# Performance work log

Measured on AMD Instinct MI355X. Metric: run time of the kernel, lower is better.

The kernel has to match this reference:

```python
import jax, jax.numpy as jnp
import numpy as np
from jax import lax

DN = ('NCHW', 'OIHW', 'NCHW')

def _conv(x, w, b, stride):
    y = lax.conv_general_dilated(x, w, (stride, stride), [(1, 1), (1, 1)], dimension_numbers=DN)
    return y + b[None, :, None, None]

def _deconv(x, w, b):
    # ConvTranspose2d(k=4, stride=2, pad=1) == conv with lhs_dilation=2, pad=k-1-p=2,
    # with w already in flipped OIHW layout.
    y = lax.conv_general_dilated(x, w, (1, 1), [(2, 2), (2, 2)], lhs_dilation=(2, 2), dimension_numbers=DN)
    return y + b[None, :, None, None]

def setup_inputs() -> dict:
    key = jax.random.key(0)
    ks = jax.random.split(key, 14)
    s = 0.05  # keep activations numerically tame
    return {
        'x':   jax.random.normal(ks[0], (16, 3, 256, 256), jnp.float32),
        'ew1': jax.random.normal(ks[1], (64, 3, 4, 4), jnp.float32) * s,
        'eb1': jax.random.normal(ks[2], (64,), jnp.float32) * s,
        'ew2': jax.random.normal(ks[3], (128, 64, 4, 4), jnp.float32) * s,
        'eb2': jax.random.normal(ks[4], (128,), jnp.float32) * s,
        'ew3': jax.random.normal(ks[5], (256, 128, 4, 4), jnp.float32) * s,
        'eb3': jax.random.normal(ks[6], (256,), jnp.float32) * s,
        'cb':  jax.random.normal(ks[7], (8192, 256), jnp.float32),
        'dw1': jax.random.normal(ks[8], (128, 256, 4, 4), jnp.float32) * s,
        'db1': jax.random.normal(ks[9], (128,), jnp.float32) * s,
        'dw2': jax.random.normal(ks[10], (64, 128, 4, 4), jnp.float32) * s,
        'db2': jax.random.normal(ks[11], (64,), jnp.float32) * s,
        'dw3': jax.random.normal(ks[12], (3, 64, 4, 4), jnp.float32) * s,
        'db3': jax.random.normal(ks[13], (3,), jnp.float32) * s,
    }

def reference(x, ew1, eb1, ew2, eb2, ew3, eb3, cb, dw1, db1, dw2, db2, dw3, db3):
    # encoder: 3 stride-2 convs with ReLU between
    h = jax.nn.relu(_conv(x, ew1, eb1, 2))
    h = jax.nn.relu(_conv(h, ew2, eb2, 2))
    feat = _conv(h, ew3, eb3, 2)                     # [B, 256, 32, 32]
    B, C, H, W = feat.shape
    flat = feat.reshape(B, C, H * W).transpose(0, 2, 1)  # [B, HW, C]
    scores = jnp.einsum('btc,kc->btk', flat, cb)     # [B, HW, K] large matrix
    indices = jnp.argmax(scores, axis=-1)            # [B, HW]
    quantized = cb[indices]                          # [B, HW, C]
    q = quantized.transpose(0, 2, 1).reshape(B, C, H, W)
    # decoder: 3 stride-2 transposed convs with ReLU between
    d = jax.nn.relu(_deconv(q, dw1, db1))
    d = jax.nn.relu(_deconv(d, dw2, db2))
    recon = _deconv(d, dw3, db3)                     # [B, 3, 256, 256]
    return recon, indices
```

## Files before the change

### kernel.cpp

```cpp
#include <hip/hip_runtime.h>
#include <hip/hip_fp16.h>
#include <cstdint>
#include <cstddef>

typedef __attribute__((ext_vector_type(8))) short short8;
typedef __attribute__((ext_vector_type(8))) _Float16 h16x8;
typedef __attribute__((ext_vector_type(4))) float f32x4;

__device__ __forceinline__ short f2bf(float x) {
  union { float f; unsigned u; } a; a.f = x;
  unsigned r = a.u + 0x7fff + ((a.u >> 16) & 1);
  return (short)(r >> 16);
}
__device__ __forceinline__ float bf2f(short s) {
  union { unsigned u; float f; } a;
  a.u = ((unsigned)(unsigned short)s) << 16; return a.f;
}
__device__ __forceinline__ void fsplit16(float v, short& h, short& l) {
  __half a = __float2half(v);
  h = (short)__half_as_ushort(a);
  l = (short)__half_as_ushort(__float2half(v - __half2float(a)));
}

__device__ __forceinline__ void ld16(const void* g, void* l) {
  __builtin_amdgcn_global_load_lds(
      (const __attribute__((address_space(1))) unsigned int*)g,
      (__attribute__((address_space(3))) unsigned int*)l, 16, 0, 0);
}

__global__ __launch_bounds__(256) void conv1_kernel(
    const float* __restrict__ x, const float* __restrict__ w,
    const float* __restrict__ bias, short* __restrict__ yh, short* __restrict__ yl)
{
  __shared__ __align__(16) float wl[64 * 48];
  __shared__ float bl[64];
  const int tid = threadIdx.x;
  for (int i = tid; i < 64 * 48; i += 256) wl[i] = w[i];
  if (tid < 64) bl[tid] = bias[tid];
  __syncthreads();
  const int n  = blockIdx.y;
  const int oh = blockIdx.x * 2 + (tid >> 7);
  const int ow = tid & 127;
  const float* xb = x + (size_t)n * 3 * 65536;
  const int ih0 = oh * 2 - 1, iw0 = ow * 2 - 1;
  float xin[48];
#pragma unroll
  for (int ic = 0; ic < 3; ++ic)
#pragma unroll
    for (int kh = 0; kh < 4; ++kh) {
      int ih = ih0 + kh;
      bool rok = (unsigned)ih < 256u;
#pragma unroll
      for (int kw = 0; kw < 4; ++kw) {
        int iw = iw0 + kw;
        xin[ic * 16 + kh * 4 + kw] =
            (rok && (unsigned)iw < 256u) ? xb[ic * 65536 + ih * 256 + iw] : 0.f;
      }
    }
  const size_t ob = ((size_t)n * 16384 + oh * 128 + ow) * 64;
  for (int g = 0; g < 8; ++g) {
    short hs[8], ls[8];
#pragma unroll
    for (int j = 0; j < 8; ++j) {
      const int oc = g * 8 + j;
      float acc = bl[oc];
      const float* wo = &wl[oc * 48];
#pragma unroll
      for (int t = 0; t < 48; ++t) acc = fmaf(wo[t], xin[t], acc);
      acc = fmaxf(acc, 0.f) * 64.f;
      fsplit16(acc, hs[j], ls[j]);
    }
    *(short8*)(yh + ob + g * 8) = *(short8*)hs;
    *(short8*)(yl + ob + g * 8) = *(short8*)ls;
  }
}

template <int COUT, int CIN>
__global__ __launch_bounds__(256) void wpack_conv(
    const float* __restrict__ w, short* __restrict__ Wh, short* __restrict__ Wl)
{
  constexpr int K = 16 * CIN;
  const int idx = blockIdx.x * 256 + threadIdx.x;
  const int oc = idx / K, k = idx - oc * K;
  const int kk = k / CIN, ic = k - kk * CIN;
  const int kh = kk >> 2, kw = kk & 3;
  float v = w[(((size_t)oc * CIN + ic) * 4 + kh) * 4 + kw] * 64.f;
  short h, l;
  fsplit16(v, h, l);
  Wh[idx] = h;
  Wl[idx] = l;
}

template <int CIN, int HIN, int COUTT, bool RELU, bool OUTF>
__global__ __launch_bounds__(256) void conv_mfma(
    const short* __restrict__ inh, const short* __restrict__ inl,
    const short* __restrict__ Wph, const short* __restrict__ Wpl,
    const float* __restrict__ bias,
    short* __restrict__ outh, short* __restrict__ outl,
    float* __restrict__ outf)
{
  constexpr int K = 16 * CIN;
  constexpr int HOUT = HIN / 2;
  constexpr int MT = 128, NPX = 128;
  constexpr int GS = (HOUT == 64) ? 6 : 5;
  constexpr int AE = 4 * MT;
  constexpr int NS = K / 32;
  constexpr float RS = 1.f / 4096.f;
  __shared__ __align__(16) short AhL[2][AE * 8];
  __shared__ __align__(16) short AlL[2][AE * 8];
  __shared__ __align__(16) float bl[MT];
  const int tid = threadIdx.x;
  const int w = tid >> 6, lane = tid & 63;
  const int wm = w >> 1, wn = w & 1;
  const int kgl = lane >> 4, cl = lane & 15;
  const int n = blockIdx.z;
  const int oc0 = blockIdx.y * MT;
  const int oh0 = blockIdx.x * (NPX / HOUT);
  if (tid < MT) bl[tid] = bias[oc0 + tid];

  f32x4 acc[4][4];
#pragma unroll
  for (int i = 0; i < 4; ++i)
#pragma unroll
    for (int j = 0; j < 4; ++j) acc[i][j] = (f32x4){0.f, 0.f, 0.f, 0.f};

  auto stageA = [&](int s, int b) {
    const int kc = s * 32;
#pragma unroll
    for (int rep = 0; rep < AE / 256; ++rep) {
      int e = rep * 256 + tid;
      int kg = e >> 7, oc_l = e & (MT - 1);
      size_t go = (size_t)(oc0 + oc_l) * K + kc + kg * 8;
      int lo = (e & ~63) * 8;
      ld16(Wph + go, &AhL[b][lo]);
      ld16(Wpl + go, &AlL[b][lo]);
    }
  };
  const h16x8 zzh = {0, 0, 0, 0, 0, 0, 0, 0};
  auto loadB = [&](int s, h16x8* bh, h16x8* blv) {
    const int kc = s * 32;
    const int kk = kc / CIN, ic0 = kc % CIN;
    const int kh = kk >> 2, kw = kk & 3;
#pragma unroll
    for (int nt = 0; nt < 4; ++nt) {
      int m = wn * 64 + nt * 16 + cl;
      int ih = 2 * (oh0 + (m >> GS)) - 1 + kh;
      int iw = 2 * (m & (HOUT - 1)) - 1 + kw;
      bool ok = ((unsigned)ih < (unsigned)HIN) && ((unsigned)iw < (unsigned)HIN);
      size_t go = ok ? ((size_t)((n * HIN + ih) * HIN + iw) * CIN + ic0 + kgl * 8)
                     : (size_t)(ic0 + kgl * 8);
      h16x8 vh = *(const h16x8*)(inh + go);
      h16x8 vl = *(const h16x8*)(inl + go);
      bh[nt] = ok ? vh : zzh;
      blv[nt] = ok ? vl : zzh;
    }
  };
  auto compute = [&](int b, const h16x8* bh, const h16x8* blv) {
    h16x8 ah[4], al[4];
#pragma unroll
    for (int mt = 0; mt < 4; ++mt) {
      int row = kgl * MT + wm * 64 + mt * 16 + cl;
      ah[mt] = *(const h16x8*)&AhL[b][row * 8];
      al[mt] = *(const h16x8*)&AlL[b][row * 8];
    }
#pragma unroll
    for (int mt = 0; mt < 4; ++mt)
#pragma unroll
      for (int nt = 0; nt < 4; ++nt) {
        acc[mt][nt] = __builtin_amdgcn_mfma_f32_16x16x32_f16(
            ah[mt], bh[nt], acc[mt][nt], 0, 0, 0);
        acc[mt][nt] = __builtin_amdgcn_mfma_f32_16x16x32_f16(
            ah[mt], blv[nt], acc[mt][nt], 0, 0, 0);
        acc[mt][nt] = __builtin_amdgcn_mfma_f32_16x16x32_f16(
            al[mt], bh[nt], acc[mt][nt], 0, 0, 0);
      }
  };

  h16x8 bhA[4], blA[4], bhB[4], blB[4];
  stageA(0, 0);
  loadB(0, bhA, blA);
  __syncthreads();
  for (int s2 = 0; s2 < NS; s2 += 2) {
    stageA(s2 + 1, 1);
    loadB(s2 + 1, bhB, blB);
    compute(0, bhA, blA);
    __syncthreads();
    if (s2 + 2 < NS) { stageA(s2 + 2, 0); loadB(s2 + 2, bhA, blA); }
    compute(1, bhB, blB);
    __syncthreads();
  }
#pragma unroll
  for (int mt = 0; mt < 4; ++mt) {
    const int oc = wm * 64 + mt * 16 + kgl * 4;
    const float4 bv = *(const float4*)&bl[oc];
#pragma unroll
    for (int nt = 0; nt < 4; ++nt) {
      const int px = wn * 64 + nt * 16 + cl;
      const int oh = oh0 + (px >> GS), ow = px & (HOUT - 1);
      const size_t ob =
          ((size_t)n * (HOUT * HOUT) + oh * HOUT + ow) * COUTT + oc0 + oc;
      float v0 = acc[mt][nt][0] * RS + bv.x;
      float v1 = acc[mt][nt][1] * RS + bv.y;
      float v2 = acc[mt][nt][2] * RS + bv.z;
      float v3 = acc[mt][nt][3] * RS + bv.w;
      if (RELU) {
        v0 = fmaxf(v0, 0.f); v1 = fmaxf(v1, 0.f);
        v2 = fmaxf(v2, 0.f); v3 = fmaxf(v3, 0.f);
      }
      if constexpr (OUTF) {
        ushort4 s;
        s.x = __half_as_ushort(__float2half(v0));
        s.y = __half_as_ushort(__float2half(v1));
        s.z = __half_as_ushort(__float2half(v2));
        s.w = __half_as_ushort(__float2half(v3));
        *(ushort4*)((unsigned short*)outh + ob) = s;
        *(float4*)(outf + ob) = make_float4(v0, v1, v2, v3);
      } else {
        short4 hh, ll;
        fsplit16(v0 * 64.f, hh.x, ll.x);
        fsplit16(v1 * 64.f, hh.y, ll.y);
        fsplit16(v2 * 64.f, hh.z, ll.z);
        fsplit16(v3 * 64.f, hh.w, ll.w);
        *(short4*)(outh + ob) = hh;
        *(short4*)(outl + ob) = ll;
      }
    }
  }
}

__global__ __launch_bounds__(256) void cb_convert(
    const float* __restrict__ cb, short* __restrict__ cbh,
    short* __restrict__ cbl, short* __restrict__ cb16)
{
  const int g = blockIdx.x * 256 + threadIdx.x;
  const float* p = cb + (size_t)g * 8;
  short hs[8], ls[8], fs[8];
#pragma unroll
  for (int u = 0; u < 8; ++u) {
    float v = p[u];
    short h = f2bf(v);
    hs[u] = h;
    ls[u] = f2bf(v - bf2f(h));
    fs[u] = (short)__half_as_ushort(__float2half(v));
  }
  *(short8*)(cbh + (size_t)g * 8) = *(short8*)hs;
  *(short8*)(cbl + (size_t)g * 8) = *(short8*)ls;
  *(short8*)(cb16 + (size_t)g * 8) = *(short8*)fs;
}

__global__ __launch_bounds__(256) void vq_mfma(
    const short* __restrict__ cb16, const short* __restrict__ ft16,
    float2* __restrict__ pval, int2* __restrict__ pidx)
{
  __shared__ __align__(16) short Ah[2][4 * 128 * 8];
  __shared__ __align__(16) short Bh[2][4 * 128 * 8];
  const int tid = threadIdx.x;
  const int w = tid >> 6, lane = tid & 63;
  const int wm = w >> 1, wn = w & 1;
  const int tg = blockIdx.x, cg = blockIdx.y;
  const int code0 = cg * 128, tok0 = tg * 128;
  const int kgl = lane >> 4, cl = lane & 15;

  f32x4 acc[4][4];
#pragma unroll
  for (int i = 0; i < 4; ++i)
#pragma unroll
    for (int j = 0; j < 4; ++j) acc[i][j] = (f32x4){0.f, 0.f, 0.f, 0.f};

  const int i0 = w * 128;
  auto stage = [&](int s, int b) {
    const int kc = s * 32;
#pragma unroll
    for (int rep = 0; rep < 2; ++rep) {
      int ib = i0 + rep * 64;
      int i = ib + lane;
      int m = i & 127, kg = i >> 7;
      size_t goffA = (size_t)(code0 + m) * 256 + kc + kg * 8;
      size_t goffB = (size_t)(tok0 + m) * 256 + kc + kg * 8;
      int loff = ib * 8;
      ld16(cb16 + goffA, &Ah[b][loff]);
      ld16(ft16 + goffB, &Bh[b][loff]);
    }
  };
  auto compute = [&](int b) {
    h16x8 ah[4], bh[4];
#pragma unroll
    for (int mt = 0; mt < 4; ++mt) {
      int row = wm * 64 + mt * 16 + cl;
      ah[mt] = *(const h16x8*)&Ah[b][(kgl * 128 + row) * 8];
    }
#pragma unroll
    for (int nt = 0; nt < 4; ++nt) {
      int row = wn * 64 + nt * 16 + cl;
      bh[nt] = *(const h16x8*)&Bh[b][(kgl * 128 + row) * 8];
    }
#pragma unroll
    for (int mt = 0; mt < 4; ++mt)
#pragma unroll
      for (int nt = 0; nt < 4; ++nt)
        acc[mt][nt] = __builtin_amdgcn_mfma_f32_16x16x32_f16(
            ah[mt], bh[nt], acc[mt][nt], 0, 0, 0);
  };

  stage(0, 0);
  __syncthreads();
  for (int s2 = 0; s2 < 8; s2 += 2) {
    stage(s2 + 1, 1);
    compute(0);
    __syncthreads();
    if (s2 + 2 < 8) stage(s2 + 2, 0);
    compute(1);
    __syncthreads();
  }

  float* Sv = (float*)&Ah[0][0];
  int* Si = (int*)&Bh[0][0];
#pragma unroll
  for (int nt = 0; nt < 4; ++nt) {
    float v1 = -3.4e38f, v2 = -3.4e38f;
    int j1 = 0, j2 = 0;
#pragma unroll
    for (int mt = 0; mt < 4; ++mt) {
      int cb2 = code0 + wm * 64 + mt * 16 + kgl * 4;
      f32x4 a = acc[mt][nt];
#pragma unroll
      for (int r = 0; r < 4; ++r) {
        float val = a[r];
        int code = cb2 + r;
        if (val > v1) { v2 = v1; j2 = j1; v1 = val; j1 = code; }
        else if (val > v2) { v2 = val; j2 = code; }
      }
    }
    for (int mk = 16; mk < 64; mk <<= 1) {
      float ov1 = __shfl_xor(v1, mk);
      int oj1 = __shfl_xor(j1, mk);
      float ov2 = __shfl_xor(v2, mk);
      int oj2 = __shfl_xor(j2, mk);
      if (ov1 > v1) {
        if (v1 >= ov2) { v2 = v1; j2 = j1; } else { v2 = ov2; j2 = oj2; }
        v1 = ov1; j1 = oj1;
      } else if (ov1 > v2) { v2 = ov1; j2 = oj1; }
    }
    if (lane < 16) {
      int tl = wn * 64 + nt * 16 + lane;
      Sv[(wm * 128 + tl) * 2 + 0] = v1;
      Sv[(wm * 128 + tl) * 2 + 1] = v2;
      Si[(wm * 128 + tl) * 2 + 0] = j1;
      Si[(wm * 128 + tl) * 2 + 1] = j2;
    }
  }
  __syncthreads();
  if (tid < 128) {
    int tl = tid;
    float v1 = Sv[tl * 2], v2 = Sv[tl * 2 + 1];
    int j1 = Si[tl * 2], j2 = Si[tl * 2 + 1];
    float ov1 = Sv[(128 + tl) * 2], ov2 = Sv[(128 + tl) * 2 + 1];
    int oj1 = Si[(128 + tl) * 2], oj2 = Si[(128 + tl) * 2 + 1];
    if (ov1 > v1) {
      if (v1 >= ov2) { v2 = v1; j2 = j1; } else { v2 = ov2; j2 = oj2; }
      v1 = ov1; j1 = oj1;
    } else if (ov1 > v2) { v2 = ov1; j2 = oj1; }
    size_t o = (size_t)cg * 16384 + tok0 + tl;
    pval[o] = make_float2(v1, v2);
    pidx[o] = make_int2(j1, j2);
  }
}

__global__ __launch_bounds__(256) void vq_rescore(
    const float2* __restrict__ pval, const int2* __restrict__ pidx,
    const float* __restrict__ featc, const float* __restrict__ cb,
    int* __restrict__ fidx, float* __restrict__ idx_out)
{
  const int t = blockIdx.x * 256 + threadIdx.x;
  float vs[4] = {-3.4e38f, -3.4e38f, -3.4e38f, -3.4e38f};
  int is[4] = {0, 0, 0, 0};
  for (int cgi = 0; cgi < 64; ++cgi) {
    float2 pv = pval[(size_t)cgi * 16384 + t];
    int2 pi = pidx[(size_t)cgi * 16384 + t];
#pragma unroll
    for (int s = 0; s < 2; ++s) {
      float v = s ? pv.y : pv.x;
      int ii = s ? pi.y : pi.x;
      if (v > vs[3]) {
        vs[3] = v; is[3] = ii;
#pragma unroll
        for (int k = 3; k > 0; --k)
          if (vs[k] > vs[k - 1]) {
            float tv = vs[k]; vs[k] = vs[k - 1]; vs[k - 1] = tv;
            int ti = is[k]; is[k] = is[k - 1]; is[k - 1] = ti;
          }
      }
    }
  }
  const float4* fc = (const float4*)(featc + (size_t)t * 256);
  const float4* c0 = (const float4*)(cb + (size_t)is[0] * 256);
  const float4* c1 = (const float4*)(cb + (size_t)is[1] * 256);
  const float4* c2 = (const float4*)(cb + (size_t)is[2] * 256);
  const float4* c3 = (const float4*)(cb + (size_t)is[3] * 256);
  float s0 = 0.f, s1 = 0.f, s2 = 0.f, s3 = 0.f;
  for (int k4 = 0; k4 < 64; ++k4) {
    float4 f = fc[k4];
    float4 w0 = c0[k4], w1 = c1[k4], w2 = c2[k4], w3 = c3[k4];
    s0 = fmaf(w0.x, f.x, fmaf(w0.y, f.y, fmaf(w0.z, f.z, fmaf(w0.w, f.w, s0))));
    s1 = fmaf(w1.x, f.x, fmaf(w1.y, f.y, fmaf(w1.z, f.z, fmaf(w1.w, f.w, s1))));
    s2 = fmaf(w2.x, f.x, fmaf(w2.y, f.y, fmaf(w2.z, f.z, fmaf(w2.w, f.w, s2))));
    s3 = fmaf(w3.x, f.x, fmaf(w3.y, f.y, fmaf(w3.z, f.z, fmaf(w3.w, f.w, s3))));
  }
  float best = s0; int bi = is[0];
  float sv[3] = {s1, s2, s3};
  int si2[3] = {is[1], is[2], is[3]};
#pragma unroll
  for (int c = 0; c < 3; ++c)
    if (sv[c] > best || (sv[c] == best && si2[c] < bi)) { best = sv[c]; bi = si2[c]; }
  fidx[t] = bi;
  idx_out[t] = (float)bi;
}

template <int COUT, int CIN>
__global__ __launch_bounds__(256) void wpack(
    const float* __restrict__ w, short* __restrict__ Ah, short* __restrict__ Al)
{
  constexpr int K = 4 * CIN;
  const int idx = blockIdx.x * 256 + threadIdx.x;
  const int par = idx / (COUT * K);
  const int rem = idx % (COUT * K);
  const int oc = rem / K;
  const int k = rem % K;
  const int kk = k / CIN, ic = k % CIN;
  const int kh = 2 * (kk >> 1) + (par >> 1);
  const int kw = 2 * (kk & 1) + (par & 1);
  float v = w[(((size_t)oc * CIN + ic) * 4 + kh) * 4 + kw];
  short h = f2bf(v);
  Ah[idx] = h;
  Al[idx] = f2bf(v - bf2f(h));
}

__global__ __launch_bounds__(256) void gather2(
    const short* __restrict__ cbh, const short* __restrict__ cbl,
    const int* __restrict__ fidx, short* __restrict__ qTh, short* __restrict__ qTl)
{
  const int tid = threadIdx.x;
  const int gt = blockIdx.x * 64 + (tid >> 2);
  const int part = tid & 3;
  const int code = fidx[gt];
  const short8* sh = (const short8*)(cbh + (size_t)code * 256 + part * 64);
  const short8* sl = (const short8*)(cbl + (size_t)code * 256 + part * 64);
  short8* dh = (short8*)(qTh + (size_t)gt * 256 + part * 64);
  short8* dl = (short8*)(qTl + (size_t)gt * 256 + part * 64);
#pragma unroll
  for (int j = 0; j < 8; ++j) { dh[j] = sh[j]; dl[j] = sl[j]; }
}

template <int CIN, int GRID, int COUT, int NPX, int WM, int WN, bool OUT_HALF>
__global__ __launch_bounds__(256) void deconv_mfma(
    const short* __restrict__ inh, const short* __restrict__ inl,
    const short* __restrict__ Aph, const short* __restrict__ Apl,
    const float* __restrict__ bias, void* __restrict__ out_h,
    void* __restrict__ out_l)
{
  constexpr int K = 4 * CIN, HOUT = 2 * GRID, AE = 4 * COUT;
  constexpr int GS = (GRID == 32) ? 5 : 6;
  constexpr int NS = K / 32;
  __shared__ __align__(16) short AhL[2][AE * 8];
  __shared__ __align__(16) short AlL[2][AE * 8];
  __shared__ float bl[COUT];
  const int tid = threadIdx.x;
  const int w = tid >> 6, lane = tid & 63;
  const int wm = w / WN, wn = w % WN;
  const int kgl = lane >> 4, cl = lane & 15;
  const int par = blockIdx.y, n = blockIdx.z;
  const int pr = par >> 1, pc = par & 1;
  const int Ut0 = blockIdx.x * (NPX / GRID);
  if (tid < COUT) bl[tid] = bias[tid];

  f32x4 acc[4][4];
#pragma unroll
  for (int i = 0; i < 4; ++i)
#pragma unroll
    for (int j = 0; j < 4; ++j) acc[i][j] = (f32x4){0.f, 0.f, 0.f, 0.f};

  auto stageA = [&](int s, int b) {
    const int kc = s * 32;
#pragma unroll
    for (int rep = 0; rep < AE / 256; ++rep) {
      int e = rep * 256 + tid;
      int kg = e / COUT, oc_l = e % COUT;
      size_t go = ((size_t)(par * COUT + oc_l)) * K + kc + kg * 8;
      int lo = (e & ~63) * 8;
      ld16(Aph + go, &AhL[b][lo]);
      ld16(Apl + go, &AlL[b][lo]);
    }
  };
  const short8 zz = {0, 0, 0, 0, 0, 0, 0, 0};
  auto loadB = [&](int s, short8* bh, short8* blo) {
    const int kc = s * 32;
    const int kk = kc / CIN, ic0 = kc % CIN;
    const int dr = (kk >> 1) + pr - 1, dc = (kk & 1) + pc - 1;
#pragma unroll
    for (int nt = 0; nt < 4; ++nt) {
      int m = wn * 64 + nt * 16 + cl;
      int sU = Ut0 + (m >> GS) + dr;
      int sV = (m & (GRID - 1)) + dc;
      bool ok = (unsigned)sU < (unsigned)GRID && (unsigned)sV < (unsigned)GRID;
      long pix = (long)(n * GRID + sU) * GRID + sV;
      size_t go = ok ? (size_t)(pix * CIN + ic0 + kgl * 8)
                     : (size_t)(ic0 + kgl * 8);
      short8 vh = *(const short8*)(inh + go);
      short8 vl = *(const short8*)(inl + go);
      bh[nt] = ok ? vh : zz;
      blo[nt] = ok ? vl : zz;
    }
  };
  auto compute = [&](int b, const short8* bh, const short8* blo) {
    short8 ah[4], al[4];
#pragma unroll
    for (int mt = 0; mt < 4; ++mt) {
      int row = kgl * COUT + wm * 64 + mt * 16 + cl;
      ah[mt] = *(const short8*)&AhL[b][row * 8];
      al[mt] = *(const short8*)&AlL[b][row * 8];
    }
#pragma unroll
    for (int mt = 0; mt < 4; ++mt)
#pragma unroll
      for (int nt = 0; nt < 4; ++nt) {
        acc[mt][nt] = __builtin_amdgcn_mfma_f32_16x16x32_bf16(
            ah[mt], bh[nt], acc[mt][nt], 0, 0, 0);
        acc[mt][nt] = __builtin_amdgcn_mfma_f32_16x16x32_bf16(
            ah[mt], blo[nt], acc[mt][nt], 0, 0, 0);
        acc[mt][nt] = __builtin_amdgcn_mfma_f32_16x16x32_bf16(
            al[mt], bh[nt], acc[mt][nt], 0, 0, 0);
      }
  };

  short8 bhA[4], blA[4], bhB[4], blB[4];
  stageA(0, 0);
  loadB(0, bhA, blA);
  __syncthreads();
  for (int s2 = 0; s2 < NS; s2 += 2) {
    stageA(s2 + 1, 1);
    loadB(s2 + 1, bhB, blB);
    compute(0, bhA, blA);
    __syncthreads();
    if (s2 + 2 < NS) { stageA(s2 + 2, 0); loadB(s2 + 2, bhA, blA); }
    compute(1, bhB, blB);
    __syncthreads();
  }
#pragma unroll
  for (int mt = 0; mt < 4; ++mt) {
    const int oc = wm * 64 + mt * 16 + kgl * 4;
    const float4 bv = *(const float4*)&bl[oc];
#pragma unroll
    for (int nt = 0; nt < 4; ++nt) {
      const int px = wn * 64 + nt * 16 + cl;
      const int U = Ut0 + (px >> GS), V = px & (GRID - 1);
      const int r = 2 * U + pr, c = 2 * V + pc;
      const size_t ob = ((size_t)n * HOUT * HOUT + (size_t)r * HOUT + c) * COUT + oc;
      float v0 = fmaxf(acc[mt][nt][0] + bv.x, 0.f);
      float v1 = fmaxf(acc[mt][nt][1] + bv.y, 0.f);
      float v2 = fmaxf(acc[mt][nt][2] + bv.z, 0.f);
      float v3 = fmaxf(acc[mt][nt][3] + bv.w, 0.f);
      if constexpr (OUT_HALF) {
        ushort4 s;
        s.x = __half_as_ushort(__float2half(v0));
        s.y = __half_as_ushort(__float2half(v1));
        s.z = __half_as_ushort(__float2half(v2));
        s.w = __half_as_ushort(__float2half(v3));
        *(ushort4*)((unsigned short*)out_h + ob) = s;
      } else {
        short4 hh, ll;
        hh.x = f2bf(v0); ll.x = f2bf(v0 - bf2f(hh.x));
        hh.y = f2bf(v1); ll.y = f2bf(v1 - bf2f(hh.y));
        hh.z = f2bf(v2); ll.z = f2bf(v2 - bf2f(hh.z));
        hh.w = f2bf(v3); ll.w = f2bf(v3 - bf2f(hh.w));
        *(short4*)((short*)out_h + ob) = hh;
        *(short4*)((short*)out_l + ob) = ll;
      }
    }
  }
}

__global__ __launch_bounds__(256) void deconv3_kernel(
    const __half* __restrict__ d2, const float* __restrict__ w,
    const float* __restrict__ bias, float* __restrict__ y)
{
  __shared__ __align__(16) float Xl[108 * 68];
  __shared__ __align__(16) float wl[4 * 4 * 3 * 64];
  const int tid = threadIdx.x;
  for (int i = tid; i < 3072; i += 256) {
    int oc = i >> 10, ic = (i >> 4) & 63, kh = (i >> 2) & 3, kw = i & 3;
    int par = (kh & 1) * 2 + (kw & 1), kidx = (kh >> 1) * 2 + (kw >> 1);
    wl[((par * 4 + kidx) * 3 + oc) * 64 + ic] = w[i];
  }
  const int n = blockIdx.z, r0 = blockIdx.y * 8, c0 = blockIdx.x * 32;
  const int gr0 = (r0 >> 1) - 1, gc0 = (c0 >> 1) - 1;
  for (int e = tid; e < 1728; e += 256) {
    int pl = e >> 4, sub = e & 15;
    int rr = pl / 18, cc = pl - rr * 18;
    int gr = gr0 + rr, gc = gc0 + cc;
    float4 v = make_float4(0.f, 0.f, 0.f, 0.f);
    if ((unsigned)gr < 128u && (unsigned)gc < 128u) {
      const __half2* p =
          (const __half2*)(d2 + ((size_t)(n * 16384 + gr * 128 + gc) * 64 + sub * 4));
      float2 f0 = __half22float2(p[0]);
      float2 f1 = __half22float2(p[1]);
      v = make_float4(f0.x, f0.y, f1.x, f1.y);
    }
    *(float4*)&Xl[pl * 68 + sub * 4] = v;
  }
  __syncthreads();
  const int wv = tid >> 6, lane = tid & 63;
  const int pr = wv >> 1, pc = wv & 1;
  const int Ul = lane >> 4, Vl = lane & 15;
  float a0 = bias[0], a1 = bias[1], a2 = bias[2];
  const int parb = wv * 768;
#pragma unroll
  for (int ic4 = 0; ic4 < 16; ++ic4) {
    float4 xv[4];
#pragma unroll
    for (int t = 0; t < 4; ++t) {
      int lr = Ul + (t >> 1) + pr, lc = Vl + (t & 1) + pc;
      xv[t] = *(const float4*)&Xl[(lr * 18 + lc) * 68 + ic4 * 4];
    }
#pragma unroll
    for (int t = 0; t < 4; ++t) {
      float4 w0 = *(const float4*)&wl[parb + (t * 3 + 0) * 64 + ic4 * 4];
      float4 w1 = *(const float4*)&wl[parb + (t * 3 + 1) * 64 + ic4 * 4];
      float4 w2 = *(const float4*)&wl[parb + (t * 3 + 2) * 64 + ic4 * 4];
      a0 = fmaf(w0.x, xv[t].x, fmaf(w0.y, xv[t].y, fmaf(w0.z, xv[t].z, fmaf(w0.w, xv[t].w, a0))));
      a1 = fmaf(w1.x, xv[t].x, fmaf(w1.y, xv[t].y, fmaf(w1.z, xv[t].z, fmaf(w1.w, xv[t].w, a1))));
      a2 = fmaf(w2.x, xv[t].x, fmaf(w2.y, xv[t].y, fmaf(w2.z, xv[t].z, fmaf(w2.w, xv[t].w, a2))));
    }
  }
  const int r = r0 + 2 * Ul + pr, c = c0 + 2 * Vl + pc;
  float* yn = y + (size_t)n * 3 * 65536 + r * 256 + c;
  yn[0] = a0;
  yn[65536] = a1;
  yn[131072] = a2;
}

extern "C" void kernel_launch(void* const* d_in, const int* in_sizes, int n_in,
                              void* d_out, int out_size, void* d_ws, size_t ws_size,
                              hipStream_t stream)
{
  const float* x   = (const float*)d_in[0];
  const float* ew1 = (const float*)d_in[1];
  const float* eb1 = (const float*)d_in[2];
  const float* ew2 = (const float*)d_in[3];
  const float* eb2 = (const float*)d_in[4];
  const float* ew3 = (const float*)d_in[5];
  const float* eb3 = (const float*)d_in[6];
  const float* cb  = (const float*)d_in[7];
  const float* dw1 = (const float*)d_in[8];
  const float* db1 = (const float*)d_in[9];
  const float* dw2 = (const float*)d_in[10];
  const float* db2 = (const float*)d_in[11];
  const float* dw3 = (const float*)d_in[12];
  const float* db3 = (const float*)d_in[13];

  float* recon = (float*)d_out;
  float* idxf  = (float*)d_out + 3145728;

  const size_t MB = 1048576ull;
  char* ws = (char*)d_ws;
  short* h1h = (short*)ws;
  short* h1l = (short*)(ws + 32 * MB);
  short* h2h = (short*)(ws + 64 * MB);
  short* h2l = (short*)(ws + 80 * MB);
  short* ft16  = (short*)ws;
  float* featf = (float*)(ws + 16 * MB);
  short* cbh  = (short*)(ws + 64 * MB);
  short* cbl  = (short*)(ws + 68 * MB);
  short* cb16 = (short*)(ws + 72 * MB);
  float2* pval = (float2*)(ws + 76 * MB);
  int2*   pidx = (int2*)(ws + 84 * MB);
  int*    fidx = (int*)(ws + 92 * MB);
  short* A1h = (short*)(ws + 76 * MB);
  short* A1l = (short*)(ws + 77 * MB);
  short* A2h = (short*)(ws + 78 * MB);
  short* A2l = (short*)(ws + 78 * MB + 262144);
  short* qTh = (short*)ws;
  short* qTl = (short*)(ws + 8 * MB);
  short* d1h = (short*)(ws + 32 * MB);
  short* d1l = (short*)(ws + 48 * MB);
  __half* d2 = (__half*)ws;
  short* W2h = (short*)recon;
  short* W2l = W2h + 131072;
  short* W3h = W2h + 262144;
  short* W3l = W2h + 786432;

  conv1_kernel<<<dim3(64, 16), 256, 0, stream>>>(x, ew1, eb1, h1h, h1l);
  wpack_conv<128, 64><<<dim3(512), 256, 0, stream>>>(ew2, W2h, W2l);
  conv_mfma<64, 128, 128, true, false><<<dim3(32, 1, 16), 256, 0, stream>>>(
      h1h, h1l, W2h, W2l, eb2, h2h, h2l, nullptr);
  wpack_conv<256, 128><<<dim3(2048), 256, 0, stream>>>(ew3, W3h, W3l);
  conv_mfma<128, 64, 256, false, true><<<dim3(8, 2, 16), 256, 0, stream>>>(
      h2h, h2l, W3h, W3l, eb3, ft16, nullptr, featf);

  cb_convert<<<dim3(1024), 256, 0, stream>>>(cb, cbh, cbl, cb16);
  vq_mfma<<<dim3(128, 64), 256, 0, stream>>>(cb16, ft16, pval, pidx);
  vq_rescore<<<dim3(64), 256, 0, stream>>>(pval, pidx, featf, cb, fidx, idxf);

  wpack<128, 256><<<dim3(2048), 256, 0, stream>>>(dw1, A1h, A1l);
  wpack<64, 128><<<dim3(512), 256, 0, stream>>>(dw2, A2h, A2l);
  gather2<<<dim3(256), 256, 0, stream>>>(cbh, cbl, fidx, qTh, qTl);

  deconv_mfma<256, 32, 128, 128, 2, 2, false>
      <<<dim3(8, 4, 16), 256, 0, stream>>>(qTh, qTl, A1h, A1l, db1, d1h, d1l);
  deconv_mfma<128, 64, 64, 256, 1, 4, true>
      <<<dim3(16, 4, 16), 256, 0, stream>>>(d1h, d1l, A2h, A2l, db2, d2, d2);
  deconv3_kernel<<<dim3(8, 32, 16), 256, 0, stream>>>(d2, dw3, db3, recon);
}
```

Measured before the change: 917.0 us.

## Loop each VQ block over eight codebook tiles and keep running top-4 candidates

The VQ scoring kernel now launches 8 codebook splits instead of 64. Each block walks 8 tiles of 128 codes with a continuous double-buffered pipeline and keeps a per-thread running top-2 across tiles. Each block emits top-4 candidates per token, and the rescore kernel merges only 8 partial lists instead of 64. This cuts partial-result traffic and merge work, and amortizes block startup and the final shuffle reduction. In exchange the grid has 1024 blocks instead of 8192, which lowers parallelism, and the per-thread top-2 could drop close candidates before rescoring.

```diff
diff --git a/kernel.cpp b/kernel.cpp
--- a/kernel.cpp
+++ b/kernel.cpp
@@ -250,25 +250,21 @@
 
 __global__ __launch_bounds__(256) void vq_mfma(
     const short* __restrict__ cb16, const short* __restrict__ ft16,
-    float2* __restrict__ pval, int2* __restrict__ pidx)
+    float4* __restrict__ t4v, int4* __restrict__ t4i)
 {
   __shared__ __align__(16) short Ah[2][4 * 128 * 8];
   __shared__ __align__(16) short Bh[2][4 * 128 * 8];
   const int tid = threadIdx.x;
   const int w = tid >> 6, lane = tid & 63;
   const int wm = w >> 1, wn = w & 1;
-  const int tg = blockIdx.x, cg = blockIdx.y;
-  const int code0 = cg * 128, tok0 = tg * 128;
+  const int tok0 = blockIdx.x * 128;
+  const int split = blockIdx.y;
   const int kgl = lane >> 4, cl = lane & 15;
-
-  f32x4 acc[4][4];
-#pragma unroll
-  for (int i = 0; i < 4; ++i)
-#pragma unroll
-    for (int j = 0; j < 4; ++j) acc[i][j] = (f32x4){0.f, 0.f, 0.f, 0.f};
-
   const int i0 = w * 128;
-  auto stage = [&](int s, int b) {
+
+  auto stage = [&](int g, int b) {
+    const int tile = g >> 3, s = g & 7;
+    const int code0 = split * 1024 + tile * 128;
     const int kc = s * 32;
 #pragma unroll
     for (int rep = 0; rep < 2; ++rep) {
@@ -282,7 +278,9 @@
       ld16(ft16 + goffB, &Bh[b][loff]);
     }
   };
-  auto compute = [&](int b) {
+
+  f32x4 acc[4][4];
+  auto compute = [&](bool first, int b) {
     h16x8 ah[4], bh[4];
 #pragma unroll
     for (int mt = 0; mt < 4; ++mt) {
@@ -294,100 +292,143 @@
       int row = wn * 64 + nt * 16 + cl;
       bh[nt] = *(const h16x8*)&Bh[b][(kgl * 128 + row) * 8];
     }
-#pragma unroll
-    for (int mt = 0; mt < 4; ++mt)
-#pragma unroll
-      for (int nt = 0; nt < 4; ++nt)
-        acc[mt][nt] = __builtin_amdgcn_mfma_f32_16x16x32_f16(
-            ah[mt], bh[nt], acc[mt][nt], 0, 0, 0);
+    if (first) {
+#pragma unroll
+      for (int mt = 0; mt < 4; ++mt)
+#pragma unroll
+        for (int nt = 0; nt < 4; ++nt)
+          acc[mt][nt] = __builtin_amdgcn_mfma_f32_16x16x32_f16(
+              ah[mt], bh[nt], (f32x4){0.f, 0.f, 0.f, 0.f}, 0, 0, 0);
+    } else {
+#pragma unroll
+      for (int mt = 0; mt < 4; ++mt)
+#pragma unroll
+        for (int nt = 0; nt < 4; ++nt)
+          acc[mt][nt] = __builtin_amdgcn_mfma_f32_16x16x32_f16(
+              ah[mt], bh[nt], acc[mt][nt], 0, 0, 0);
+    }
   };
+
+  float sv1[4], sv2[4];
+  int sj1[4], sj2[4];
+#pragma unroll
+  for (int nt = 0; nt < 4; ++nt) {
+    sv1[nt] = -3.4e38f; sv2[nt] = -3.4e38f; sj1[nt] = 0; sj2[nt] = 0;
+  }
 
   stage(0, 0);
   __syncthreads();
-  for (int s2 = 0; s2 < 8; s2 += 2) {
-    stage(s2 + 1, 1);
-    compute(0);
+  for (int g = 0; g < 64; ++g) {
+    if (g + 1 < 64) stage(g + 1, (g + 1) & 1);
+    compute((g & 7) == 0, g & 1);
+    if ((g & 7) == 7) {
+      const int tile = g >> 3;
+      const int cb2base = split * 1024 + tile * 128 + wm * 64 + kgl * 4;
+#pragma unroll
+      for (int nt = 0; nt < 4; ++nt)
+#pragma unroll
+        for (int mt = 0; mt < 4; ++mt)
+#pragma unroll
+          for (int r = 0; r < 4; ++r) {
+            float v = acc[mt][nt][r];
+            int code = cb2base + mt * 16 + r;
+            bool g1 = v > sv1[nt];
+            bool g2 = v > sv2[nt];
+            float nv2 = g1 ? sv1[nt] : (g2 ? v : sv2[nt]);
+            int nj2 = g1 ? sj1[nt] : (g2 ? code : sj2[nt]);
+            sv1[nt] = g1 ? v : sv1[nt];
+            sj1[nt] = g1 ? code : sj1[nt];
+            sv2[nt] = nv2; sj2[nt] = nj2;
+          }
+    }
     __syncthreads();
-    if (s2 + 2 < 8) stage(s2 + 2, 0);
-    compute(1);
-    __syncthreads();
-  }
-
-  float* Sv = (float*)&Ah[0][0];
-  int* Si = (int*)&Bh[0][0];
+  }
+
+  float* MrgV = (float*)&Ah[0][0];
+  int* MrgI = (int*)&Bh[0][0];
 #pragma unroll
   for (int nt = 0; nt < 4; ++nt) {
-    float v1 = -3.4e38f, v2 = -3.4e38f;
-    int j1 = 0, j2 = 0;
-#pragma unroll
-    for (int mt = 0; mt < 4; ++mt) {
-      int cb2 = code0 + wm * 64 + mt * 16 + kgl * 4;
-      f32x4 a = acc[mt][nt];
-#pragma unroll
-      for (int r = 0; r < 4; ++r) {
-        float val = a[r];
-        int code = cb2 + r;
-        if (val > v1) { v2 = v1; j2 = j1; v1 = val; j1 = code; }
-        else if (val > v2) { v2 = val; j2 = code; }
-      }
-    }
-    for (int mk = 16; mk < 64; mk <<= 1) {
-      float ov1 = __shfl_xor(v1, mk);
-      int oj1 = __shfl_xor(j1, mk);
-      float ov2 = __shfl_xor(v2, mk);
-      int oj2 = __shfl_xor(j2, mk);
-      if (ov1 > v1) {
-        if (v1 >= ov2) { v2 = v1; j2 = j1; } else { v2 = ov2; j2 = oj2; }
-        v1 = ov1; j1 = oj1;
-      } else if (ov1 > v2) { v2 = ov1; j2 = oj1; }
+    float mv[4] = {sv1[nt], sv2[nt], -3.4e38f, -3.4e38f};
+    int mj[4] = {sj1[nt], sj2[nt], 0, 0};
+#pragma unroll
+    for (int st = 16; st < 64; st <<= 1) {
+      float ov[4]; int oj[4];
+#pragma unroll
+      for (int k = 0; k < 4; ++k) {
+        ov[k] = __shfl_xor(mv[k], st);
+        oj[k] = __shfl_xor(mj[k], st);
+      }
+#pragma unroll
+      for (int k = 0; k < 4; ++k) {
+        if (ov[k] > mv[3]) {
+          mv[3] = ov[k]; mj[3] = oj[k];
+#pragma unroll
+          for (int q = 3; q > 0; --q)
+            if (mv[q] > mv[q - 1]) {
+              float tv = mv[q]; mv[q] = mv[q - 1]; mv[q - 1] = tv;
+              int tj = mj[q]; mj[q] = mj[q - 1]; mj[q - 1] = tj;
+            }
+        }
+      }
     }
     if (lane < 16) {
-      int tl = wn * 64 + nt * 16 + lane;
-      Sv[(wm * 128 + tl) * 2 + 0] = v1;
-      Sv[(wm * 128 + tl) * 2 + 1] = v2;
-      Si[(wm * 128 + tl) * 2 + 0] = j1;
-      Si[(wm * 128 + tl) * 2 + 1] = j2;
+      int tl = wn * 64 + nt * 16 + cl;
+#pragma unroll
+      for (int k = 0; k < 4; ++k) {
+        MrgV[(wm * 128 + tl) * 4 + k] = mv[k];
+        MrgI[(wm * 128 + tl) * 4 + k] = mj[k];
+      }
     }
   }
   __syncthreads();
   if (tid < 128) {
     int tl = tid;
-    float v1 = Sv[tl * 2], v2 = Sv[tl * 2 + 1];
-    int j1 = Si[tl * 2], j2 = Si[tl * 2 + 1];
-    float ov1 = Sv[(128 + tl) * 2], ov2 = Sv[(128 + tl) * 2 + 1];
-    int oj1 = Si[(128 + tl) * 2], oj2 = Si[(128 + tl) * 2 + 1];
-    if (ov1 > v1) {
-      if (v1 >= ov2) { v2 = v1; j2 = j1; } else { v2 = ov2; j2 = oj2; }
-      v1 = ov1; j1 = oj1;
-    } else if (ov1 > v2) { v2 = ov1; j2 = oj1; }
-    size_t o = (size_t)cg * 16384 + tok0 + tl;
-    pval[o] = make_float2(v1, v2);
-    pidx[o] = make_int2(j1, j2);
+    float mv[4]; int mj[4];
+#pragma unroll
+    for (int k = 0; k < 4; ++k) { mv[k] = MrgV[tl * 4 + k]; mj[k] = MrgI[tl * 4 + k]; }
+#pragma unroll
+    for (int k = 0; k < 4; ++k) {
+      float ov = MrgV[(128 + tl) * 4 + k];
+      int oj = MrgI[(128 + tl) * 4 + k];
+      if (ov > mv[3]) {
+        mv[3] = ov; mj[3] = oj;
+#pragma unroll
+        for (int q = 3; q > 0; --q)
+          if (mv[q] > mv[q - 1]) {
+            float tv = mv[q]; mv[q] = mv[q - 1]; mv[q - 1] = tv;
+            int tj = mj[q]; mj[q] = mj[q - 1]; mj[q - 1] = tj;
+          }
+      }
+    }
+    size_t o = (size_t)split * 16384 + tok0 + tl;
+    t4v[o] = make_float4(mv[0], mv[1], mv[2], mv[3]);
+    t4i[o] = make_int4(mj[0], mj[1], mj[2], mj[3]);
   }
 }
 
 __global__ __launch_bounds__(256) void vq_rescore(
-    const float2* __restrict__ pval, const int2* __restrict__ pidx,
+    const float4* __restrict__ t4v, const int4* __restrict__ t4i,
     const float* __restrict__ featc, const float* __restrict__ cb,
     int* __restrict__ fidx, float* __restrict__ idx_out)
 {
   const int t = blockIdx.x * 256 + threadIdx.x;
   float vs[4] = {-3.4e38f, -3.4e38f, -3.4e38f, -3.4e38f};
   int is[4] = {0, 0, 0, 0};
-  for (int cgi = 0; cgi < 64; ++cgi) {
-    float2 pv = pval[(size_t)cgi * 16384 + t];
-    int2 pi = pidx[(size_t)cgi * 16384 + t];
-#pragma unroll
-    for (int s = 0; s < 2; ++s) {
-      float v = s ? pv.y : pv.x;
-      int ii = s ? pi.y : pi.x;
-      if (v > vs[3]) {
-        vs[3] = v; is[3] = ii;
-#pragma unroll
-        for (int k = 3; k > 0; --k)
-          if (vs[k] > vs[k - 1]) {
-            float tv = vs[k]; vs[k] = vs[k - 1]; vs[k - 1] = tv;
-            int ti = is[k]; is[k] = is[k - 1]; is[k - 1] = ti;
+#pragma unroll
+  for (int sp = 0; sp < 8; ++sp) {
+    float4 v4 = t4v[(size_t)sp * 16384 + t];
+    int4 i4 = t4i[(size_t)sp * 16384 + t];
+    float vv[4] = {v4.x, v4.y, v4.z, v4.w};
+    int ii[4] = {i4.x, i4.y, i4.z, i4.w};
+#pragma unroll
+    for (int k = 0; k < 4; ++k) {
+      if (vv[k] > vs[3]) {
+        vs[3] = vv[k]; is[3] = ii[k];
+#pragma unroll
+        for (int q = 3; q > 0; --q)
+          if (vs[q] > vs[q - 1]) {
+            float tv = vs[q]; vs[q] = vs[q - 1]; vs[q - 1] = tv;
+            int ti = is[q]; is[q] = is[q - 1]; is[q - 1] = ti;
           }
       }
     }
@@ -671,8 +712,8 @@
   short* cbh  = (short*)(ws + 64 * MB);
   short* cbl  = (short*)(ws + 68 * MB);
   short* cb16 = (short*)(ws + 72 * MB);
-  float2* pval = (float2*)(ws + 76 * MB);
-  int2*   pidx = (int2*)(ws + 84 * MB);
+  float4* t4v = (float4*)(ws + 80 * MB);
+  int4*   t4i = (int4*)(ws + 82 * MB);
   int*    fidx = (int*)(ws + 92 * MB);
   short* A1h = (short*)(ws + 76 * MB);
   short* A1l = (short*)(ws + 77 * MB);
@@ -697,8 +738,8 @@
       h2h, h2l, W3h, W3l, eb3, ft16, nullptr, featf);
 
   cb_convert<<<dim3(1024), 256, 0, stream>>>(cb, cbh, cbl, cb16);
-  vq_mfma<<<dim3(128, 64), 256, 0, stream>>>(cb16, ft16, pval, pidx);
-  vq_rescore<<<dim3(64), 256, 0, stream>>>(pval, pidx, featf, cb, fidx, idxf);
+  vq_mfma<<<dim3(128, 8), 256, 0, stream>>>(cb16, ft16, t4v, t4i);
+  vq_rescore<<<dim3(64), 256, 0, stream>>>(t4v, t4i, featf, cb, fidx, idxf);
 
   wpack<128, 256><<<dim3(2048), 256, 0, stream>>>(dw1, A1h, A1l);
   wpack<64, 128><<<dim3(512), 256, 0, stream>>>(dw2, A2h, A2l);
```

New measurement: 916.4 us. About the same (-0.1%).
